# Kernel tuning notes

Measured on AMD Instinct MI355X. Metric: run time of the kernel, lower is better.

Reference implementation:

```python
import jax, jax.numpy as jnp
import numpy as np

# Fixed hierarchical grouping of the 15 regions into 5 groups of 3 (from split_regions)
SPLIT_IDX = np.array([[0, 1, 8], [2, 4, 6], [3, 5, 7], [9, 11, 13], [10, 12, 14]])
BN_EPS = 1e-5


def _bn_relu(x, g, b):
    # BatchNorm over (batch, spatial) dims in training-stats mode, then ReLU
    mu = jnp.mean(x, axis=(0, 2, 3), keepdims=True)
    var = jnp.var(x, axis=(0, 2, 3), keepdims=True)
    xn = (x - mu) * jax.lax.rsqrt(var + BN_EPS)
    return jax.nn.relu(xn * g[None, :, None, None] + b[None, :, None, None])


def _local_agg(x, params):
    # x: [B, Cin, G, K]; pointwise conv (1x1) -> BN -> ReLU per layer, then max over K
    for W, g, b in params:
        x = jnp.einsum('oi,bigk->bogk', W, x)
        x = _bn_relu(x, g, b)
    return jnp.max(x, axis=-1)  # [B, Cout, G]


def setup_inputs() -> dict:
    key = jax.random.key(0)
    ks = jax.random.split(key, 8)
    B, G, K = 32, 15, 2048
    inp = {"local_regions": jax.random.normal(ks[0], (B, G, K, 3), jnp.float32)}
    chans = [(3, 64, 64), (67, 128, 128), (131, 256, 256)]
    ki = 1
    for li, (c0, c1, c2) in enumerate(chans):
        for wi, (co, ci) in enumerate([(c1, c0), (c2, c1)]):
            inp[f"la{li}_w{wi}"] = jax.random.normal(ks[ki], (co, ci), jnp.float32) * (1.0 / np.sqrt(ci))
            inp[f"la{li}_g{wi}"] = jnp.ones((co,), jnp.float32)
            inp[f"la{li}_b{wi}"] = jnp.zeros((co,), jnp.float32)
            ki += 1
    return inp


def reference(local_regions,
              la0_w0, la0_g0, la0_b0, la0_w1, la0_g1, la0_b1,
              la1_w0, la1_g0, la1_b0, la1_w1, la1_g1, la1_b1,
              la2_w0, la2_g0, la2_b0, la2_w1, la2_g1, la2_b1):
    la0 = [(la0_w0, la0_g0, la0_b0), (la0_w1, la0_g1, la0_b1)]
    la1 = [(la1_w0, la1_g0, la1_b0), (la1_w1, la1_g1, la1_b1)]
    la2 = [(la2_w0, la2_g0, la2_b0), (la2_w1, la2_g1, la2_b1)]
    idx = jnp.asarray(SPLIT_IDX)

    x = jnp.transpose(local_regions, (0, 3, 1, 2))  # [B, 3, 15, K]
    centroids_1 = jnp.mean(x, axis=-1)              # [B, 3, 15]
    relative_1 = x - centroids_1[..., None]
    lf1 = _local_agg(relative_1, la0)               # [B, 64, 15]
    local_features = jnp.concatenate([centroids_1, lf1], axis=1)  # [B, 67, 15]

    # level 2: regroup 15 regions into [5, 3]
    lf1_s = jnp.transpose(lf1, (0, 2, 1))[:, idx, :]         # [B, 5, 3, 64]
    lr2 = jnp.transpose(centroids_1, (0, 2, 1))[:, idx, :]   # [B, 5, 3, 3]
    c2 = jnp.mean(lr2, axis=2)                               # [B, 5, 3]
    rel2 = lr2 - c2[:, :, None, :]
    feats2 = jnp.concatenate([rel2, lf1_s], axis=-1)         # [B, 5, 3, 67]
    feats2 = jnp.transpose(feats2, (0, 3, 1, 2))             # [B, 67, 5, 3]
    lf2 = _local_agg(feats2, la1)                            # [B, 128, 5]

    # level 3: global
    c3 = jnp.mean(c2, axis=1)                                # [B, 3]
    rel3 = c2 - c3[:, None, :]                               # [B, 5, 3]
    lf2 = jnp.concatenate([jnp.transpose(rel3, (0, 2, 1)), lf2], axis=1)  # [B, 131, 5]
    lf2 = lf2[:, :, None, :]                                 # [B, 131, 1, 5]
    gf = _local_agg(lf2, la2)                                # [B, 256, 1]
    return gf.squeeze(2), local_features
```

## Files before the change

kernel.cpp:

```cpp
#include <hip/hip_runtime.h>
#include <math.h>

#define BB 32
#define GG 15
#define KK 2048
#define NB 480
#define N1F 983040.0f
#define EPS 1e-5f
#define PZN ((int)0xAAAAAAAA)

typedef _Float16 half8 __attribute__((ext_vector_type(8)));
typedef float f32x4 __attribute__((ext_vector_type(4)));

#define WS_CENT  0
#define WS_MN    1920
#define GSREL    63360
#define GBN1     63600
#define G2A      67440
#define G2B      67952
#define G3A      68464
#define G3B      69488
#define FSREL    70512
#define FBN1     70520
#define F2A      70648
#define F2B      70904
#define F3A      71160
#define F3B      71672
#define CNT_GRP  72184
#define CNT_SUP  72376
#define CNT_DONE 72382

#define SMEMF 7936

__device__ const int SIDX[15] = {0,1,8, 2,4,6, 3,5,7, 9,11,13, 10,12,14};

__device__ __forceinline__ float wave_sum(float v){
    for (int off = 32; off; off >>= 1) v += __shfl_down(v, off, 64);
    return v;
}
__device__ __forceinline__ float aloadf(const float* p){
    return __hip_atomic_load(p, __ATOMIC_RELAXED, __HIP_MEMORY_SCOPE_AGENT);
}
__device__ __forceinline__ int aloadi(const int* p){
    return __hip_atomic_load(p, __ATOMIC_RELAXED, __HIP_MEMORY_SCOPE_AGENT);
}
template<int SLP, class Fold>
__device__ __forceinline__ void gbar(int* wsi, int idx, int gi, int ngrp,
                                     int* sflag, Fold fold){
    __syncthreads();
    if (threadIdx.x == 0)
        sflag[0] = (atomicAdd(&wsi[CNT_GRP + idx*32 + gi], 1) == PZN + 15) ? 1 : 0;
    __syncthreads();
    if (sflag[0]) {
        if (threadIdx.x == 0)
            sflag[1] = (atomicAdd(&wsi[CNT_SUP + idx], 1) == PZN + ngrp - 1) ? 1 : 0;
        __syncthreads();
        if (sflag[1]) {
            fold();
            __syncthreads();
            if (threadIdx.x == 0) atomicExch(&wsi[CNT_DONE + idx], 1);
        }
    }
    if (threadIdx.x == 0) {
        int g = 0;
        while (aloadi(&wsi[CNT_DONE + idx]) != 1 && ++g < 4000000)
            __builtin_amdgcn_s_sleep(SLP);
    }
    __syncthreads();
    asm volatile("" ::: "memory");
}

__global__ void __launch_bounds__(256, 2) mega(
        const float* __restrict__ x,
        const float* __restrict__ w00, const float* __restrict__ g00, const float* __restrict__ b00,
        const float* __restrict__ w01, const float* __restrict__ g01, const float* __restrict__ b01,
        const float* __restrict__ w10, const float* __restrict__ g10, const float* __restrict__ b10,
        const float* __restrict__ w11, const float* __restrict__ g11, const float* __restrict__ b11,
        const float* __restrict__ w20, const float* __restrict__ g20, const float* __restrict__ b20,
        const float* __restrict__ w21, const float* __restrict__ g21, const float* __restrict__ b21,
        float* __restrict__ ws, float* __restrict__ out) {
    __shared__ __align__(16) float smemf[SMEMF];
    float* xls  = smemf;
    float* redM = smemf + 6144; float* redN = smemf + 6400;
    float* redS = smemf + 6656; float* redQ = smemf + 6912;
    float* bcast= smemf + 7168;
    int*   sflag= (int*)(smemf + 7916);
    float* s1ls  = smemf;
    float* t1ls  = smemf + 64;
    float* centls= smemf + 128;
    float* c2ls  = smemf + 176;
    float* c3ls  = smemf + 192;
    float* f2ls  = smemf + 256;
    float* vls   = smemf + 1280;
    float* f3ls  = smemf + 3200;
    float* u3ls  = smemf + 3968;
    int* wsi = (int*)ws;

    int bid = blockIdx.x, tid = threadIdx.x;
    int b_ = bid / GG, g_ = bid % GG;
    int wv = tid >> 6, lane = tid & 63, l15 = lane & 15, quad = lane >> 4;
    int gi = bid >> 4;

    {
        const float4* xp4 = (const float4*)(x + (size_t)bid * KK * 3);
        float4* xls4 = (float4*)xls;
        #pragma unroll
        for (int i = 0; i < 6; i++) xls4[i*256 + tid] = xp4[i*256 + tid];
        __syncthreads();
        float m[9] = {0,0,0,0,0,0,0,0,0};
        float a[24];
        const float* bp = &xls[tid*24];
        #pragma unroll
        for (int i = 0; i < 6; i++)
            *reinterpret_cast<float4*>(&a[i*4]) = *reinterpret_cast<const float4*>(&bp[i*4]);
        #pragma unroll
        for (int p = 0; p < 8; p++) {
            float ax=a[p*3], ay=a[p*3+1], az=a[p*3+2];
            m[0]+=ax; m[1]+=ay; m[2]+=az;
            m[3]=fmaf(ax,ax,m[3]); m[4]=fmaf(ay,ay,m[4]); m[5]=fmaf(az,az,m[5]);
            m[6]=fmaf(ax,ay,m[6]); m[7]=fmaf(ax,az,m[7]); m[8]=fmaf(ay,az,m[8]);
        }
        #pragma unroll
        for (int q = 0; q < 9; q++) {
            float v = wave_sum(m[q]);
            if (lane == 0) redM[q*4 + wv] = v;
        }
        __syncthreads();
        if (tid == 0) {
            float t[9];
            #pragma unroll
            for (int q = 0; q < 9; q++) t[q] = redM[q*4]+redM[q*4+1]+redM[q*4+2]+redM[q*4+3];
            float c0 = t[0]/KK, c1 = t[1]/KK, c2 = t[2]/KK;
            bcast[0]=c0; bcast[1]=c1; bcast[2]=c2;
            out[8192 + b_*(67*GG) + 0*GG + g_] = c0;
            out[8192 + b_*(67*GG) + 1*GG + g_] = c1;
            out[8192 + b_*(67*GG) + 2*GG + g_] = c2;
            atomicExch(&ws[WS_CENT + bid*4 + 0], c0);
            atomicExch(&ws[WS_CENT + bid*4 + 1], c1);
            atomicExch(&ws[WS_CENT + bid*4 + 2], c2);
            redM[40] = t[3] - KK*c0*c0;  redM[41] = t[4] - KK*c1*c1;
            redM[42] = t[5] - KK*c2*c2;  redM[43] = t[6] - KK*c0*c1;
            redM[44] = t[7] - KK*c0*c2;  redM[45] = t[8] - KK*c1*c2;
        }
        __syncthreads();
    }
    if (tid < 6) atomicAdd(&ws[GSREL + gi*8 + tid], redM[40 + tid]);

    half8 afA[4], afB[4];
    #pragma unroll
    for (int t = 0; t < 4; t++)
        #pragma unroll
        for (int j = 0; j < 8; j++) {
            afA[t][j] = (_Float16)w01[(t*16 + l15)*64 + quad*8 + j];
            afB[t][j] = (_Float16)w01[(t*16 + l15)*64 + 32 + quad*8 + j];
        }
    gbar<8>(wsi, 0, gi, 30, sflag, [&]{
        if (tid < 6) {
            float acc = 0.f;
            #pragma unroll
            for (int s = 0; s < 30; s++) acc += aloadf(&ws[GSREL + s*8 + tid]);
            atomicExch(&ws[FSREL + tid], acc);
        }
    });

    if (tid < 6) bcast[3+tid] = aloadf(&ws[FSREL + tid]) / N1F;
    __syncthreads();
    float c0 = bcast[0], c1 = bcast[1], c2v = bcast[2];
    float S00=bcast[3], S11=bcast[4], S22=bcast[5], S01=bcast[6], S02=bcast[7], S12=bcast[8];

    float wa0[8], wa1[8], wa2[8], ba[8], wb0[8], wb1[8], wb2[8], bb[8];
    #pragma unroll
    for (int j = 0; j < 8; j++) {
        int cA = quad*8 + j;
        float u0=w00[cA*3+0], u1=w00[cA*3+1], u2=w00[cA*3+2];
        float var = u0*u0*S00 + u1*u1*S11 + u2*u2*S22
                  + 2.f*(u0*u1*S01 + u0*u2*S02 + u1*u2*S12);
        float a1 = g00[cA]*rsqrtf(var + EPS);
        wa0[j]=a1*u0; wa1[j]=a1*u1; wa2[j]=a1*u2; ba[j]=b00[cA];
        int cB = cA + 32;
        float v0=w00[cB*3+0], v1=w00[cB*3+1], v2=w00[cB*3+2];
        float varB = v0*v0*S00 + v1*v1*S11 + v2*v2*S22
                   + 2.f*(v0*v1*S01 + v0*v2*S02 + v1*v2*S12);
        float a1B = g00[cB]*rsqrtf(varB + EPS);
        wb0[j]=a1B*v0; wb1[j]=a1B*v1; wb2[j]=a1B*v2; bb[j]=b00[cB];
    }
    float mx[16], mn[16], sm[16], sq[16];
    #pragma unroll
    for (int s = 0; s < 16; s++) { mx[s]=-1e30f; mn[s]=1e30f; sm[s]=0.f; sq[s]=0.f; }

    for (int it = 0; it < 32; it++) {
        int k = it*64 + wv*16 + l15;
        float r0 = xls[k*3+0]-c0, r1 = xls[k*3+1]-c1, r2 = xls[k*3+2]-c2v;
        half8 bf0, bf1;
        #pragma unroll
        for (int j = 0; j < 8; j++) {
            float pA = fmaf(wa0[j],r0, fmaf(wa1[j],r1, fmaf(wa2[j],r2, ba[j])));
            bf0[j] = (_Float16)fmaxf(pA, 0.f);
            float pB = fmaf(wb0[j],r0, fmaf(wb1[j],r1, fmaf(wb2[j],r2, bb[j])));
            bf1[j] = (_Float16)fmaxf(pB, 0.f);
        }
        #pragma unroll
        for (int t = 0; t < 4; t++) {
            f32x4 acc = {0.f,0.f,0.f,0.f};
            acc = __builtin_amdgcn_mfma_f32_16x16x32_f16(afA[t], bf0, acc, 0, 0, 0);
            acc = __builtin_amdgcn_mfma_f32_16x16x32_f16(afB[t], bf1, acc, 0, 0, 0);
            #pragma unroll
            for (int r = 0; r < 4; r++) {
                float h = acc[r];
                int s = t*4 + r;
                mx[s]=fmaxf(mx[s],h); mn[s]=fminf(mn[s],h);
                sm[s]+=h;             sq[s]=fmaf(h,h,sq[s]);
            }
        }
    }
    #pragma unroll
    for (int m = 1; m < 16; m <<= 1) {
        #pragma unroll
        for (int s = 0; s < 16; s++) {
            mx[s] = fmaxf(mx[s], __shfl_xor(mx[s], m, 64));
            mn[s] = fminf(mn[s], __shfl_xor(mn[s], m, 64));
            sm[s] += __shfl_xor(sm[s], m, 64);
            sq[s] += __shfl_xor(sq[s], m, 64);
        }
    }
    __syncthreads();
    if (l15 == 0) {
        #pragma unroll
        for (int t = 0; t < 4; t++)
            #pragma unroll
            for (int r = 0; r < 4; r++) {
                int o = t*16 + quad*4 + r;
                redM[wv*64+o]=mx[t*4+r]; redN[wv*64+o]=mn[t*4+r];
                redS[wv*64+o]=sm[t*4+r]; redQ[wv*64+o]=sq[t*4+r];
            }
    }
    __syncthreads();
    float Mreg = -1e30f, Nreg = 1e30f;
    if (tid < 64) {
        float S=0.f, Q=0.f;
        #pragma unroll
        for (int w = 0; w < 4; w++) {
            Mreg = fmaxf(Mreg, redM[w*64+tid]); Nreg = fminf(Nreg, redN[w*64+tid]);
            S += redS[w*64+tid];               Q += redQ[w*64+tid];
        }
        atomicAdd(&ws[GBN1 + gi*128 + tid], S);
        atomicAdd(&ws[GBN1 + gi*128 + 64 + tid], Q);
        atomicExch(&ws[WS_MN + bid*128 + tid], Mreg);
        atomicExch(&ws[WS_MN + bid*128 + 64 + tid], Nreg);
    }
    gbar<8>(wsi, 1, gi, 30, sflag, [&]{
        if (tid < 128) {
            float acc = 0.f;
            #pragma unroll
            for (int s = 0; s < 30; s++) acc += aloadf(&ws[GBN1 + s*128 + tid]);
            atomicExch(&ws[FBN1 + tid], acc);
        }
    });

    if (tid < 64) {
        float SM = aloadf(&ws[FBN1 + tid]);
        float SQ = aloadf(&ws[FBN1 + 64 + tid]);
        float mean = SM / N1F;
        float var  = SQ / N1F - mean*mean;
        float s1 = g01[tid]*rsqrtf(var + EPS);
        float t1 = b01[tid] - mean*s1;
        float val = fmaxf(fmaf(s1, (s1 >= 0.f) ? Mreg : Nreg, t1), 0.f);
        out[8192 + b_*(67*GG) + (3+tid)*GG + g_] = val;
        s1ls[tid] = s1; t1ls[tid] = t1;
    }
    if (g_ != 0) return;

    int git = b_ >> 4;
    if (tid < 45) centls[tid] = aloadf(&ws[WS_CENT + (b_*GG + tid/3)*4 + tid%3]);
    __syncthreads();
    if (tid < 15) {
        int s = tid/3, i = tid%3;
        c2ls[tid] = (centls[SIDX[s*3+0]*3+i] + centls[SIDX[s*3+1]*3+i]
                   + centls[SIDX[s*3+2]*3+i]) * (1.f/3.f);
    }
    __syncthreads();
    if (tid < 3)
        c3ls[tid] = (c2ls[tid]+c2ls[3+tid]+c2ls[6+tid]+c2ls[9+tid]+c2ls[12+tid]) * 0.2f;
    if (tid < 45) {
        int p = tid/3, i = tid%3;
        f2ls[p*68 + i] = centls[SIDX[p]*3+i] - c2ls[(p/3)*3 + i];
    }
    for (int u = tid; u < 960; u += 256) {
        int p = u >> 6, ch = u & 63, gsrc = SIDX[p];
        float Mv = aloadf(&ws[WS_MN + (b_*GG + gsrc)*128 + ch]);
        float Nv = aloadf(&ws[WS_MN + (b_*GG + gsrc)*128 + 64 + ch]);
        float s1 = s1ls[ch], t1 = t1ls[ch];
        f2ls[p*68 + 3 + ch] = fmaxf(fmaf(s1, (s1 >= 0.f) ? Mv : Nv, t1), 0.f);
    }
    __syncthreads();

    int half = tid >> 7, oc = tid & 127, pbase = half*8, npts = 8 - half;
    float acc[8];
    #pragma unroll
    for (int q = 0; q < 8; q++) acc[q] = 0.f;
    {
        const float* wr = w10 + oc*67;
        #pragma unroll 4
        for (int c = 0; c < 67; c++) {
            float wv_ = wr[c];
            #pragma unroll
            for (int q = 0; q < 8; q++)
                acc[q] = fmaf(wv_, f2ls[(pbase+q)*68 + c], acc[q]);
        }
        float S = 0.f, Q = 0.f;
        #pragma unroll
        for (int q = 0; q < 8; q++) if (q < npts) { S += acc[q]; Q = fmaf(acc[q],acc[q],Q); }
        redS[tid] = S; redQ[tid] = Q;
        __syncthreads();
        if (tid < 128) {
            atomicAdd(&ws[G2A + git*256 + tid],       redS[tid] + redS[tid+128]);
            atomicAdd(&ws[G2A + git*256 + 128 + tid], redQ[tid] + redQ[tid+128]);
        }
    }
    gbar<2>(wsi, 2, git, 2, sflag, [&]{
        float a = aloadf(&ws[G2A + tid]) + aloadf(&ws[G2A + 256 + tid]);
        atomicExch(&ws[F2A + tid], a);
    });

    {
        float mean = aloadf(&ws[F2A + oc]) / 480.f;
        float var  = aloadf(&ws[F2A + 128 + oc]) / 480.f - mean*mean;
        float s2 = g10[oc]*rsqrtf(var + EPS), t2 = b10[oc] - mean*s2;
        #pragma unroll
        for (int q = 0; q < 8; q++) {
            float v = fmaxf(fmaf(s2, acc[q], t2), 0.f);
            if (q < npts) vls[(pbase+q)*128 + oc] = v;
        }
    }
    __syncthreads();
    #pragma unroll
    for (int q = 0; q < 8; q++) acc[q] = 0.f;
    {
        const float* wr = w11 + oc*128;
        #pragma unroll 4
        for (int c = 0; c < 128; c++) {
            float wv_ = wr[c];
            #pragma unroll
            for (int q = 0; q < 8; q++)
                acc[q] = fmaf(wv_, vls[(pbase+q)*128 + c], acc[q]);
        }
        float S = 0.f, Q = 0.f;
        #pragma unroll
        for (int q = 0; q < 8; q++) if (q < npts) { S += acc[q]; Q = fmaf(acc[q],acc[q],Q); }
        redS[tid] = S; redQ[tid] = Q;
        __syncthreads();
        if (tid < 128) {
            atomicAdd(&ws[G2B + git*256 + tid],       redS[tid] + redS[tid+128]);
            atomicAdd(&ws[G2B + git*256 + 128 + tid], redQ[tid] + redQ[tid+128]);
        }
    }
    gbar<2>(wsi, 3, git, 2, sflag, [&]{
        float a = aloadf(&ws[G2B + tid]) + aloadf(&ws[G2B + 256 + tid]);
        atomicExch(&ws[F2B + tid], a);
    });

    {
        float mean = aloadf(&ws[F2B + oc]) / 480.f;
        float var  = aloadf(&ws[F2B + 128 + oc]) / 480.f - mean*mean;
        float s3 = g11[oc]*rsqrtf(var + EPS), t3 = b11[oc] - mean*s3;
        #pragma unroll
        for (int q = 0; q < 8; q++) {
            float v = fmaxf(fmaf(s3, acc[q], t3), 0.f);
            if (q < npts) vls[(pbase+q)*128 + oc] = v;
        }
    }
    __syncthreads();
    for (int u = tid; u < 640; u += 256) {
        int s = u >> 7, o2 = u & 127;
        float m = fmaxf(fmaxf(vls[(3*s)*128+o2], vls[(3*s+1)*128+o2]),
                        vls[(3*s+2)*128+o2]);
        f3ls[s*132 + 3 + o2] = m;
    }
    if (tid < 15) {
        int s = tid/3, i = tid%3;
        f3ls[s*132 + i] = c2ls[tid] - c3ls[i];
    }
    __syncthreads();

    float a3[5];
    #pragma unroll
    for (int s = 0; s < 5; s++) a3[s] = 0.f;
    {
        const float* wr = w20 + tid*131;
        #pragma unroll 4
        for (int c = 0; c < 131; c++) {
            float wv_ = wr[c];
            #pragma unroll
            for (int s = 0; s < 5; s++)
                a3[s] = fmaf(wv_, f3ls[s*132 + c], a3[s]);
        }
        float S = 0.f, Q = 0.f;
        #pragma unroll
        for (int s = 0; s < 5; s++) { S += a3[s]; Q = fmaf(a3[s],a3[s],Q); }
        atomicAdd(&ws[G3A + git*512 + tid], S);
        atomicAdd(&ws[G3A + git*512 + 256 + tid], Q);
    }
    gbar<2>(wsi, 4, git, 2, sflag, [&]{
        float a0 = aloadf(&ws[G3A + tid])       + aloadf(&ws[G3A + 512 + tid]);
        float a1 = aloadf(&ws[G3A + 256 + tid]) + aloadf(&ws[G3A + 512 + 256 + tid]);
        atomicExch(&ws[F3A + tid], a0);
        atomicExch(&ws[F3A + 256 + tid], a1);
    });

    {
        float mean = aloadf(&ws[F3A + tid]) / 160.f;
        float var  = aloadf(&ws[F3A + 256 + tid]) / 160.f - mean*mean;
        float s4 = g20[tid]*rsqrtf(var + EPS), t4 = b20[tid] - mean*s4;
        #pragma unroll
        for (int s = 0; s < 5; s++)
            u3ls[s*256 + tid] = fmaxf(fmaf(s4, a3[s], t4), 0.f);
    }
    __syncthreads();
    #pragma unroll
    for (int s = 0; s < 5; s++) a3[s] = 0.f;
    {
        const float* wr = w21 + tid*256;
        #pragma unroll 4
        for (int c = 0; c < 256; c++) {
            float wv_ = wr[c];
            #pragma unroll
            for (int s = 0; s < 5; s++)
                a3[s] = fmaf(wv_, u3ls[s*256 + c], a3[s]);
        }
        float S = 0.f, Q = 0.f;
        #pragma unroll
        for (int s = 0; s < 5; s++) { S += a3[s]; Q = fmaf(a3[s],a3[s],Q); }
        atomicAdd(&ws[G3B + git*512 + tid], S);
        atomicAdd(&ws[G3B + git*512 + 256 + tid], Q);
    }
    gbar<2>(wsi, 5, git, 2, sflag, [&]{
        float a0 = aloadf(&ws[G3B + tid])       + aloadf(&ws[G3B + 512 + tid]);
        float a1 = aloadf(&ws[G3B + 256 + tid]) + aloadf(&ws[G3B + 512 + 256 + tid]);
        atomicExch(&ws[F3B + tid], a0);
        atomicExch(&ws[F3B + 256 + tid], a1);
    });

    {
        float mean = aloadf(&ws[F3B + tid]) / 160.f;
        float var  = aloadf(&ws[F3B + 256 + tid]) / 160.f - mean*mean;
        float s5 = g21[tid]*rsqrtf(var + EPS), t5 = b21[tid] - mean*s5;
        float m = -1e30f;
        #pragma unroll
        for (int s = 0; s < 5; s++)
            m = fmaxf(m, fmaxf(fmaf(s5, a3[s], t5), 0.f));
        out[b_*256 + tid] = m;
    }
}

extern "C" void kernel_launch(void* const* d_in, const int* in_sizes, int n_in,
                              void* d_out, int out_size, void* d_ws, size_t ws_size,
                              hipStream_t stream) {
    (void)in_sizes; (void)n_in; (void)out_size; (void)ws_size;
    const float* x   = (const float*)d_in[0];
    const float* w00 = (const float*)d_in[1];
    const float* g00 = (const float*)d_in[2];
    const float* b00 = (const float*)d_in[3];
    const float* w01 = (const float*)d_in[4];
    const float* g01 = (const float*)d_in[5];
    const float* b01 = (const float*)d_in[6];
    const float* w10 = (const float*)d_in[7];
    const float* g10 = (const float*)d_in[8];
    const float* b10 = (const float*)d_in[9];
    const float* w11 = (const float*)d_in[10];
    const float* g11 = (const float*)d_in[11];
    const float* b11 = (const float*)d_in[12];
    const float* w20 = (const float*)d_in[13];
    const float* g20 = (const float*)d_in[14];
    const float* b20 = (const float*)d_in[15];
    const float* w21 = (const float*)d_in[16];
    const float* g21 = (const float*)d_in[17];
    const float* b21 = (const float*)d_in[18];
    float* out = (float*)d_out;
    float* ws  = (float*)d_ws;

    mega<<<NB, 256, 0, stream>>>(x, w00,g00,b00, w01,g01,b01, w10,g10,b10,
                                 w11,g11,b11, w20,g20,b20, w21,g21,b21, ws, out);
}
```

Baseline: 191.1 us.

## Split persistent megakernel with spin barriers into chain of stream-ordered kernels

Replaces the single persistent kernel, which used atomic counters and spin-wait grid barriers between BatchNorm stages, with eight separate kernel launches. Global statistics are now written as per-block partials and reduced deterministically by the next kernel, with no atomics. Level-2/3 activations are stored in the workspace and recomputed or reloaded across launches. This removes spin-barrier latency and atomic contention at the cost of several extra launch overheads and redundant recomputation, such as re-reading x and recomputing level-2 features.

```diff
diff --git a/kernel.cpp b/kernel.cpp
--- a/kernel.cpp
+++ b/kernel.cpp
@@ -1,36 +1,27 @@
 #include <hip/hip_runtime.h>
 #include <math.h>
 
-#define BB 32
 #define GG 15
 #define KK 2048
 #define NB 480
 #define N1F 983040.0f
 #define EPS 1e-5f
-#define PZN ((int)0xAAAAAAAA)
 
 typedef _Float16 half8 __attribute__((ext_vector_type(8)));
 typedef float f32x4 __attribute__((ext_vector_type(4)));
 
-#define WS_CENT  0
-#define WS_MN    1920
-#define GSREL    63360
-#define GBN1     63600
-#define G2A      67440
-#define G2B      67952
-#define G3A      68464
-#define G3B      69488
-#define FSREL    70512
-#define FBN1     70520
-#define F2A      70648
-#define F2B      70904
-#define F3A      71160
-#define F3B      71672
-#define CNT_GRP  72184
-#define CNT_SUP  72376
-#define CNT_DONE 72382
-
-#define SMEMF 7936
+#define CENT  0
+#define MOM   1920
+#define SELO  5760
+#define SQ1   36480
+#define H2BO  36480
+#define H3AO  97920
+#define H3BO  5760
+#define P2A   138880
+#define P2B   147072
+#define P3A   155264
+#define P3B   171648
+#define COEF1 188032
 
 __device__ const int SIDX[15] = {0,1,8, 2,4,6, 3,5,7, 9,11,13, 10,12,14};
 
@@ -38,114 +29,86 @@
     for (int off = 32; off; off >>= 1) v += __shfl_down(v, off, 64);
     return v;
 }
-__device__ __forceinline__ float aloadf(const float* p){
-    return __hip_atomic_load(p, __ATOMIC_RELAXED, __HIP_MEMORY_SCOPE_AGENT);
-}
-__device__ __forceinline__ int aloadi(const int* p){
-    return __hip_atomic_load(p, __ATOMIC_RELAXED, __HIP_MEMORY_SCOPE_AGENT);
-}
-template<int SLP, class Fold>
-__device__ __forceinline__ void gbar(int* wsi, int idx, int gi, int ngrp,
-                                     int* sflag, Fold fold){
-    __syncthreads();
-    if (threadIdx.x == 0)
-        sflag[0] = (atomicAdd(&wsi[CNT_GRP + idx*32 + gi], 1) == PZN + 15) ? 1 : 0;
-    __syncthreads();
-    if (sflag[0]) {
-        if (threadIdx.x == 0)
-            sflag[1] = (atomicAdd(&wsi[CNT_SUP + idx], 1) == PZN + ngrp - 1) ? 1 : 0;
-        __syncthreads();
-        if (sflag[1]) {
-            fold();
-            __syncthreads();
-            if (threadIdx.x == 0) atomicExch(&wsi[CNT_DONE + idx], 1);
-        }
-    }
-    if (threadIdx.x == 0) {
-        int g = 0;
-        while (aloadi(&wsi[CNT_DONE + idx]) != 1 && ++g < 4000000)
-            __builtin_amdgcn_s_sleep(SLP);
-    }
-    __syncthreads();
-    asm volatile("" ::: "memory");
-}
-
-__global__ void __launch_bounds__(256, 2) mega(
+
+__global__ __launch_bounds__(256) void k1_moments(
+        const float* __restrict__ x, float* __restrict__ ws, float* __restrict__ out){
+    __shared__ __align__(16) float xls[6144];
+    __shared__ float red[40];
+    int bid = blockIdx.x, tid = threadIdx.x;
+    int b_ = bid / GG, g_ = bid % GG;
+    int wv = tid >> 6, lane = tid & 63;
+    const float4* xp4 = (const float4*)(x + (size_t)bid * KK * 3);
+    float4* xls4 = (float4*)xls;
+    #pragma unroll
+    for (int i = 0; i < 6; i++) xls4[i*256 + tid] = xp4[i*256 + tid];
+    __syncthreads();
+    float m[9] = {0,0,0,0,0,0,0,0,0};
+    float a[24];
+    const float* bp = &xls[tid*24];
+    #pragma unroll
+    for (int i = 0; i < 6; i++)
+        *reinterpret_cast<float4*>(&a[i*4]) = *reinterpret_cast<const float4*>(&bp[i*4]);
+    #pragma unroll
+    for (int p = 0; p < 8; p++) {
+        float ax=a[p*3], ay=a[p*3+1], az=a[p*3+2];
+        m[0]+=ax; m[1]+=ay; m[2]+=az;
+        m[3]=fmaf(ax,ax,m[3]); m[4]=fmaf(ay,ay,m[4]); m[5]=fmaf(az,az,m[5]);
+        m[6]=fmaf(ax,ay,m[6]); m[7]=fmaf(ax,az,m[7]); m[8]=fmaf(ay,az,m[8]);
+    }
+    #pragma unroll
+    for (int q = 0; q < 9; q++) {
+        float v = wave_sum(m[q]);
+        if (lane == 0) red[q*4 + wv] = v;
+    }
+    __syncthreads();
+    if (tid == 0) {
+        float t[9];
+        #pragma unroll
+        for (int q = 0; q < 9; q++) t[q] = red[q*4]+red[q*4+1]+red[q*4+2]+red[q*4+3];
+        float c0 = t[0]/KK, c1 = t[1]/KK, c2 = t[2]/KK;
+        out[8192 + b_*1005 + 0*GG + g_] = c0;
+        out[8192 + b_*1005 + 1*GG + g_] = c1;
+        out[8192 + b_*1005 + 2*GG + g_] = c2;
+        ws[CENT + bid*4 + 0] = c0;
+        ws[CENT + bid*4 + 1] = c1;
+        ws[CENT + bid*4 + 2] = c2;
+        ws[MOM + bid*8 + 0] = t[3] - KK*c0*c0;
+        ws[MOM + bid*8 + 1] = t[4] - KK*c1*c1;
+        ws[MOM + bid*8 + 2] = t[5] - KK*c2*c2;
+        ws[MOM + bid*8 + 3] = t[6] - KK*c0*c1;
+        ws[MOM + bid*8 + 4] = t[7] - KK*c0*c2;
+        ws[MOM + bid*8 + 5] = t[8] - KK*c1*c2;
+    }
+}
+
+__global__ __launch_bounds__(256, 2) void k3_mfma(
         const float* __restrict__ x,
-        const float* __restrict__ w00, const float* __restrict__ g00, const float* __restrict__ b00,
-        const float* __restrict__ w01, const float* __restrict__ g01, const float* __restrict__ b01,
-        const float* __restrict__ w10, const float* __restrict__ g10, const float* __restrict__ b10,
-        const float* __restrict__ w11, const float* __restrict__ g11, const float* __restrict__ b11,
-        const float* __restrict__ w20, const float* __restrict__ g20, const float* __restrict__ b20,
-        const float* __restrict__ w21, const float* __restrict__ g21, const float* __restrict__ b21,
-        float* __restrict__ ws, float* __restrict__ out) {
-    __shared__ __align__(16) float smemf[SMEMF];
+        const float* __restrict__ w00, const float* __restrict__ g00,
+        const float* __restrict__ b00, const float* __restrict__ w01,
+        const float* __restrict__ g01, float* __restrict__ ws){
+    __shared__ __align__(16) float smemf[7440];
     float* xls  = smemf;
     float* redM = smemf + 6144; float* redN = smemf + 6400;
     float* redS = smemf + 6656; float* redQ = smemf + 6912;
     float* bcast= smemf + 7168;
-    int*   sflag= (int*)(smemf + 7916);
-    float* s1ls  = smemf;
-    float* t1ls  = smemf + 64;
-    float* centls= smemf + 128;
-    float* c2ls  = smemf + 176;
-    float* c3ls  = smemf + 192;
-    float* f2ls  = smemf + 256;
-    float* vls   = smemf + 1280;
-    float* f3ls  = smemf + 3200;
-    float* u3ls  = smemf + 3968;
-    int* wsi = (int*)ws;
+    float* sred = smemf + 7184;
 
     int bid = blockIdx.x, tid = threadIdx.x;
-    int b_ = bid / GG, g_ = bid % GG;
     int wv = tid >> 6, lane = tid & 63, l15 = lane & 15, quad = lane >> 4;
-    int gi = bid >> 4;
 
     {
         const float4* xp4 = (const float4*)(x + (size_t)bid * KK * 3);
         float4* xls4 = (float4*)xls;
         #pragma unroll
         for (int i = 0; i < 6; i++) xls4[i*256 + tid] = xp4[i*256 + tid];
-        __syncthreads();
-        float m[9] = {0,0,0,0,0,0,0,0,0};
-        float a[24];
-        const float* bp = &xls[tid*24];
-        #pragma unroll
-        for (int i = 0; i < 6; i++)
-            *reinterpret_cast<float4*>(&a[i*4]) = *reinterpret_cast<const float4*>(&bp[i*4]);
-        #pragma unroll
-        for (int p = 0; p < 8; p++) {
-            float ax=a[p*3], ay=a[p*3+1], az=a[p*3+2];
-            m[0]+=ax; m[1]+=ay; m[2]+=az;
-            m[3]=fmaf(ax,ax,m[3]); m[4]=fmaf(ay,ay,m[4]); m[5]=fmaf(az,az,m[5]);
-            m[6]=fmaf(ax,ay,m[6]); m[7]=fmaf(ax,az,m[7]); m[8]=fmaf(ay,az,m[8]);
-        }
-        #pragma unroll
-        for (int q = 0; q < 9; q++) {
-            float v = wave_sum(m[q]);
-            if (lane == 0) redM[q*4 + wv] = v;
-        }
-        __syncthreads();
-        if (tid == 0) {
-            float t[9];
-            #pragma unroll
-            for (int q = 0; q < 9; q++) t[q] = redM[q*4]+redM[q*4+1]+redM[q*4+2]+redM[q*4+3];
-            float c0 = t[0]/KK, c1 = t[1]/KK, c2 = t[2]/KK;
-            bcast[0]=c0; bcast[1]=c1; bcast[2]=c2;
-            out[8192 + b_*(67*GG) + 0*GG + g_] = c0;
-            out[8192 + b_*(67*GG) + 1*GG + g_] = c1;
-            out[8192 + b_*(67*GG) + 2*GG + g_] = c2;
-            atomicExch(&ws[WS_CENT + bid*4 + 0], c0);
-            atomicExch(&ws[WS_CENT + bid*4 + 1], c1);
-            atomicExch(&ws[WS_CENT + bid*4 + 2], c2);
-            redM[40] = t[3] - KK*c0*c0;  redM[41] = t[4] - KK*c1*c1;
-            redM[42] = t[5] - KK*c2*c2;  redM[43] = t[6] - KK*c0*c1;
-            redM[44] = t[7] - KK*c0*c2;  redM[45] = t[8] - KK*c1*c2;
-        }
-        __syncthreads();
-    }
-    if (tid < 6) atomicAdd(&ws[GSREL + gi*8 + tid], redM[40 + tid]);
-
+    }
+    float sacc = 0.f;
+    {
+        int c = tid >> 3, q = tid & 7;
+        #pragma unroll
+        for (int i = 0; i < 15; i++) sacc += ws[MOM + (c*15 + i)*8 + q];
+    }
+    float cload = (tid < 3) ? ws[CENT + bid*4 + tid] : 0.f;
     half8 afA[4], afB[4];
     #pragma unroll
     for (int t = 0; t < 4; t++)
@@ -154,16 +117,15 @@
             afA[t][j] = (_Float16)w01[(t*16 + l15)*64 + quad*8 + j];
             afB[t][j] = (_Float16)w01[(t*16 + l15)*64 + 32 + quad*8 + j];
         }
-    gbar<8>(wsi, 0, gi, 30, sflag, [&]{
-        if (tid < 6) {
-            float acc = 0.f;
-            #pragma unroll
-            for (int s = 0; s < 30; s++) acc += aloadf(&ws[GSREL + s*8 + tid]);
-            atomicExch(&ws[FSREL + tid], acc);
-        }
-    });
-
-    if (tid < 6) bcast[3+tid] = aloadf(&ws[FSREL + tid]) / N1F;
+    sred[tid] = sacc;
+    __syncthreads();
+    if (tid < 6) {
+        float tot = 0.f;
+        #pragma unroll
+        for (int c = 0; c < 32; c++) tot += sred[c*8 + tid];
+        bcast[3 + tid] = tot / N1F;
+    }
+    if (tid < 3) bcast[tid] = cload;
     __syncthreads();
     float c0 = bcast[0], c1 = bcast[1], c2v = bcast[2];
     float S00=bcast[3], S11=bcast[4], S22=bcast[5], S01=bcast[6], S02=bcast[7], S12=bcast[8];
@@ -224,7 +186,7 @@
         }
     }
     __syncthreads();
-    if (l15 == 0) {
+    if ((lane & 15) == 0) {
         #pragma unroll
         for (int t = 0; t < 4; t++)
             #pragma unroll
@@ -235,65 +197,140 @@
             }
     }
     __syncthreads();
-    float Mreg = -1e30f, Nreg = 1e30f;
     if (tid < 64) {
-        float S=0.f, Q=0.f;
+        float Mreg = -1e30f, Nreg = 1e30f, S=0.f, Q=0.f;
         #pragma unroll
         for (int w = 0; w < 4; w++) {
             Mreg = fmaxf(Mreg, redM[w*64+tid]); Nreg = fminf(Nreg, redN[w*64+tid]);
             S += redS[w*64+tid];               Q += redQ[w*64+tid];
         }
-        atomicAdd(&ws[GBN1 + gi*128 + tid], S);
-        atomicAdd(&ws[GBN1 + gi*128 + 64 + tid], Q);
-        atomicExch(&ws[WS_MN + bid*128 + tid], Mreg);
-        atomicExch(&ws[WS_MN + bid*128 + 64 + tid], Nreg);
-    }
-    gbar<8>(wsi, 1, gi, 30, sflag, [&]{
-        if (tid < 128) {
-            float acc = 0.f;
-            #pragma unroll
-            for (int s = 0; s < 30; s++) acc += aloadf(&ws[GBN1 + s*128 + tid]);
-            atomicExch(&ws[FBN1 + tid], acc);
-        }
-    });
-
+        ws[SELO + bid*64 + tid] = (g01[tid] >= 0.f) ? Mreg : Nreg;
+        ws[SQ1 + bid*128 + tid] = S;
+        ws[SQ1 + bid*128 + 64 + tid] = Q;
+    }
+}
+
+__global__ __launch_bounds__(256) void k_bn1red(
+        const float* __restrict__ g01, const float* __restrict__ b01,
+        float* __restrict__ ws){
+    __shared__ float sm[256];
+    int tid = threadIdx.x;
+    int e = tid & 127, h = tid >> 7;
+    float acc = 0.f;
+    #pragma unroll 8
+    for (int i = 0; i < 240; i++) acc += ws[SQ1 + (h*240 + i)*128 + e];
+    sm[tid] = acc;
+    __syncthreads();
     if (tid < 64) {
-        float SM = aloadf(&ws[FBN1 + tid]);
-        float SQ = aloadf(&ws[FBN1 + 64 + tid]);
-        float mean = SM / N1F;
-        float var  = SQ / N1F - mean*mean;
+        float S = sm[tid] + sm[128 + tid];
+        float Q = sm[64 + tid] + sm[192 + tid];
+        float mean = S / N1F;
+        float var  = Q / N1F - mean*mean;
         float s1 = g01[tid]*rsqrtf(var + EPS);
         float t1 = b01[tid] - mean*s1;
-        float val = fmaxf(fmaf(s1, (s1 >= 0.f) ? Mreg : Nreg, t1), 0.f);
-        out[8192 + b_*(67*GG) + (3+tid)*GG + g_] = val;
-        s1ls[tid] = s1; t1ls[tid] = t1;
-    }
-    if (g_ != 0) return;
-
-    int git = b_ >> 4;
-    if (tid < 45) centls[tid] = aloadf(&ws[WS_CENT + (b_*GG + tid/3)*4 + tid%3]);
+        ws[COEF1 + tid] = s1;
+        ws[COEF1 + 64 + tid] = t1;
+    }
+}
+
+__global__ __launch_bounds__(256) void k_t1(
+        const float* __restrict__ w10, float* __restrict__ ws,
+        float* __restrict__ out){
+    __shared__ float s1t1[128];
+    __shared__ float cent[48];
+    __shared__ float c2[16];
+    __shared__ __align__(16) float f2[16*68];
+    __shared__ float red[512];
+    int b = blockIdx.x, tid = threadIdx.x;
+    if (tid < 128) s1t1[tid] = ws[COEF1 + tid];
+    if (tid < 45) cent[tid] = ws[CENT + (b*GG + tid/3)*4 + tid%3];
+    if (tid >= 188) f2[15*68 + (tid - 188)] = 0.f;
     __syncthreads();
     if (tid < 15) {
         int s = tid/3, i = tid%3;
-        c2ls[tid] = (centls[SIDX[s*3+0]*3+i] + centls[SIDX[s*3+1]*3+i]
-                   + centls[SIDX[s*3+2]*3+i]) * (1.f/3.f);
-    }
-    __syncthreads();
-    if (tid < 3)
-        c3ls[tid] = (c2ls[tid]+c2ls[3+tid]+c2ls[6+tid]+c2ls[9+tid]+c2ls[12+tid]) * 0.2f;
+        c2[tid] = (cent[SIDX[s*3+0]*3+i] + cent[SIDX[s*3+1]*3+i]
+                 + cent[SIDX[s*3+2]*3+i]) * (1.f/3.f);
+    }
+    __syncthreads();
     if (tid < 45) {
         int p = tid/3, i = tid%3;
-        f2ls[p*68 + i] = centls[SIDX[p]*3+i] - c2ls[(p/3)*3 + i];
+        f2[p*68 + i] = cent[SIDX[p]*3+i] - c2[(p/3)*3 + i];
     }
     for (int u = tid; u < 960; u += 256) {
-        int p = u >> 6, ch = u & 63, gsrc = SIDX[p];
-        float Mv = aloadf(&ws[WS_MN + (b_*GG + gsrc)*128 + ch]);
-        float Nv = aloadf(&ws[WS_MN + (b_*GG + gsrc)*128 + 64 + ch]);
-        float s1 = s1ls[ch], t1 = t1ls[ch];
-        f2ls[p*68 + 3 + ch] = fmaxf(fmaf(s1, (s1 >= 0.f) ? Mv : Nv, t1), 0.f);
-    }
-    __syncthreads();
-
+        int p = u >> 6, ch = u & 63, g = SIDX[p];
+        float sel = ws[SELO + (b*GG + g)*64 + ch];
+        float val = fmaxf(fmaf(s1t1[ch], sel, s1t1[64+ch]), 0.f);
+        f2[p*68 + 3 + ch] = val;
+        out[8192 + b*1005 + (3+ch)*GG + g] = val;
+    }
+    __syncthreads();
+    int half = tid >> 7, oc = tid & 127, pbase = half*8, npts = 8 - half;
+    float acc[8];
+    #pragma unroll
+    for (int q = 0; q < 8; q++) acc[q] = 0.f;
+    const float* wr = w10 + oc*67;
+    #pragma unroll 4
+    for (int c = 0; c < 67; c++) {
+        float wv_ = wr[c];
+        #pragma unroll
+        for (int q = 0; q < 8; q++)
+            acc[q] = fmaf(wv_, f2[(pbase+q)*68 + c], acc[q]);
+    }
+    float S = 0.f, Q = 0.f;
+    #pragma unroll
+    for (int q = 0; q < 8; q++) if (q < npts) { S += acc[q]; Q = fmaf(acc[q],acc[q],Q); }
+    red[tid] = S; red[256 + tid] = Q;
+    __syncthreads();
+    if (tid < 128) {
+        ws[P2A + b*256 + tid]       = red[tid] + red[128 + tid];
+        ws[P2A + b*256 + 128 + tid] = red[256 + tid] + red[256 + 128 + tid];
+    }
+}
+
+__global__ __launch_bounds__(256) void k_t2(
+        const float* __restrict__ w10, const float* __restrict__ g10,
+        const float* __restrict__ b10, const float* __restrict__ w11,
+        float* __restrict__ ws){
+    __shared__ float s1t1[128];
+    __shared__ float cent[48];
+    __shared__ float c2[16];
+    __shared__ __align__(16) float f2[16*68];
+    __shared__ __align__(16) float vls[16*128];
+    __shared__ float c2s[128], c2t[128];
+    __shared__ float red[512];
+    int b = blockIdx.x, tid = threadIdx.x;
+    if (tid < 128) {
+        float S = 0.f, Q = 0.f;
+        #pragma unroll
+        for (int i = 0; i < 32; i++) {
+            S += ws[P2A + i*256 + tid];
+            Q += ws[P2A + i*256 + 128 + tid];
+        }
+        float mean = S / 480.f, var = Q / 480.f - mean*mean;
+        float s2 = g10[tid]*rsqrtf(var + EPS);
+        c2s[tid] = s2; c2t[tid] = b10[tid] - mean*s2;
+        s1t1[tid] = ws[COEF1 + tid];
+        vls[15*128 + tid] = 0.f;
+    }
+    if (tid < 45) cent[tid] = ws[CENT + (b*GG + tid/3)*4 + tid%3];
+    if (tid >= 188) f2[15*68 + (tid - 188)] = 0.f;
+    __syncthreads();
+    if (tid < 15) {
+        int s = tid/3, i = tid%3;
+        c2[tid] = (cent[SIDX[s*3+0]*3+i] + cent[SIDX[s*3+1]*3+i]
+                 + cent[SIDX[s*3+2]*3+i]) * (1.f/3.f);
+    }
+    __syncthreads();
+    if (tid < 45) {
+        int p = tid/3, i = tid%3;
+        f2[p*68 + i] = cent[SIDX[p]*3+i] - c2[(p/3)*3 + i];
+    }
+    for (int u = tid; u < 960; u += 256) {
+        int p = u >> 6, ch = u & 63, g = SIDX[p];
+        float sel = ws[SELO + (b*GG + g)*64 + ch];
+        f2[p*68 + 3 + ch] = fmaxf(fmaf(s1t1[ch], sel, s1t1[64+ch]), 0.f);
+    }
+    __syncthreads();
     int half = tid >> 7, oc = tid & 127, pbase = half*8, npts = 8 - half;
     float acc[8];
     #pragma unroll
@@ -305,27 +342,11 @@
             float wv_ = wr[c];
             #pragma unroll
             for (int q = 0; q < 8; q++)
-                acc[q] = fmaf(wv_, f2ls[(pbase+q)*68 + c], acc[q]);
-        }
-        float S = 0.f, Q = 0.f;
-        #pragma unroll
-        for (int q = 0; q < 8; q++) if (q < npts) { S += acc[q]; Q = fmaf(acc[q],acc[q],Q); }
-        redS[tid] = S; redQ[tid] = Q;
-        __syncthreads();
-        if (tid < 128) {
-            atomicAdd(&ws[G2A + git*256 + tid],       redS[tid] + redS[tid+128]);
-            atomicAdd(&ws[G2A + git*256 + 128 + tid], redQ[tid] + redQ[tid+128]);
-        }
-    }
-    gbar<2>(wsi, 2, git, 2, sflag, [&]{
-        float a = aloadf(&ws[G2A + tid]) + aloadf(&ws[G2A + 256 + tid]);
-        atomicExch(&ws[F2A + tid], a);
-    });
-
+                acc[q] = fmaf(wv_, f2[(pbase+q)*68 + c], acc[q]);
+        }
+    }
     {
-        float mean = aloadf(&ws[F2A + oc]) / 480.f;
-        float var  = aloadf(&ws[F2A + 128 + oc]) / 480.f - mean*mean;
-        float s2 = g10[oc]*rsqrtf(var + EPS), t2 = b10[oc] - mean*s2;
+        float s2 = c2s[oc], t2 = c2t[oc];
         #pragma unroll
         for (int q = 0; q < 8; q++) {
             float v = fmaxf(fmaf(s2, acc[q], t2), 0.f);
@@ -333,123 +354,175 @@
         }
     }
     __syncthreads();
-    #pragma unroll
-    for (int q = 0; q < 8; q++) acc[q] = 0.f;
+    float acc2[8];
+    #pragma unroll
+    for (int q = 0; q < 8; q++) acc2[q] = 0.f;
     {
-        const float* wr = w11 + oc*128;
-        #pragma unroll 4
-        for (int c = 0; c < 128; c++) {
-            float wv_ = wr[c];
+        const float4* w4 = (const float4*)(w11 + oc*128);
+        #pragma unroll 2
+        for (int c4 = 0; c4 < 32; c4++) {
+            float4 wv4 = w4[c4];
+            int cb = c4*4;
             #pragma unroll
-            for (int q = 0; q < 8; q++)
-                acc[q] = fmaf(wv_, vls[(pbase+q)*128 + c], acc[q]);
-        }
+            for (int q = 0; q < 8; q++) {
+                const float* vrow = &vls[(pbase+q)*128];
+                acc2[q] = fmaf(wv4.x, vrow[cb+0], acc2[q]);
+                acc2[q] = fmaf(wv4.y, vrow[cb+1], acc2[q]);
+                acc2[q] = fmaf(wv4.z, vrow[cb+2], acc2[q]);
+                acc2[q] = fmaf(wv4.w, vrow[cb+3], acc2[q]);
+            }
+        }
+    }
+    float S = 0.f, Q = 0.f;
+    #pragma unroll
+    for (int q = 0; q < 8; q++) if (q < npts) {
+        ws[H2BO + b*1920 + (pbase+q)*128 + oc] = acc2[q];
+        S += acc2[q]; Q = fmaf(acc2[q],acc2[q],Q);
+    }
+    red[tid] = S; red[256 + tid] = Q;
+    __syncthreads();
+    if (tid < 128) {
+        ws[P2B + b*256 + tid]       = red[tid] + red[128 + tid];
+        ws[P2B + b*256 + 128 + tid] = red[256 + tid] + red[256 + 128 + tid];
+    }
+}
+
+__global__ __launch_bounds__(256) void k_t3(
+        const float* __restrict__ g11, const float* __restrict__ b11,
+        const float* __restrict__ w20, float* __restrict__ ws){
+    __shared__ float s3[128], t3[128];
+    __shared__ float cent[48];
+    __shared__ float c2[16], c3[4];
+    __shared__ __align__(16) float f3[5*132];
+    int b = blockIdx.x, tid = threadIdx.x;
+    if (tid < 128) {
         float S = 0.f, Q = 0.f;
         #pragma unroll
-        for (int q = 0; q < 8; q++) if (q < npts) { S += acc[q]; Q = fmaf(acc[q],acc[q],Q); }
-        redS[tid] = S; redQ[tid] = Q;
-        __syncthreads();
-        if (tid < 128) {
-            atomicAdd(&ws[G2B + git*256 + tid],       redS[tid] + redS[tid+128]);
-            atomicAdd(&ws[G2B + git*256 + 128 + tid], redQ[tid] + redQ[tid+128]);
-        }
-    }
-    gbar<2>(wsi, 3, git, 2, sflag, [&]{
-        float a = aloadf(&ws[G2B + tid]) + aloadf(&ws[G2B + 256 + tid]);
-        atomicExch(&ws[F2B + tid], a);
-    });
-
-    {
-        float mean = aloadf(&ws[F2B + oc]) / 480.f;
-        float var  = aloadf(&ws[F2B + 128 + oc]) / 480.f - mean*mean;
-        float s3 = g11[oc]*rsqrtf(var + EPS), t3 = b11[oc] - mean*s3;
-        #pragma unroll
-        for (int q = 0; q < 8; q++) {
-            float v = fmaxf(fmaf(s3, acc[q], t3), 0.f);
-            if (q < npts) vls[(pbase+q)*128 + oc] = v;
-        }
-    }
-    __syncthreads();
-    for (int u = tid; u < 640; u += 256) {
-        int s = u >> 7, o2 = u & 127;
-        float m = fmaxf(fmaxf(vls[(3*s)*128+o2], vls[(3*s+1)*128+o2]),
-                        vls[(3*s+2)*128+o2]);
-        f3ls[s*132 + 3 + o2] = m;
-    }
+        for (int i = 0; i < 32; i++) {
+            S += ws[P2B + i*256 + tid];
+            Q += ws[P2B + i*256 + 128 + tid];
+        }
+        float mean = S / 480.f, var = Q / 480.f - mean*mean;
+        float sv = g11[tid]*rsqrtf(var + EPS);
+        s3[tid] = sv; t3[tid] = b11[tid] - mean*sv;
+    }
+    if (tid < 45) cent[tid] = ws[CENT + (b*GG + tid/3)*4 + tid%3];
+    __syncthreads();
     if (tid < 15) {
         int s = tid/3, i = tid%3;
-        f3ls[s*132 + i] = c2ls[tid] - c3ls[i];
-    }
-    __syncthreads();
-
+        c2[tid] = (cent[SIDX[s*3+0]*3+i] + cent[SIDX[s*3+1]*3+i]
+                 + cent[SIDX[s*3+2]*3+i]) * (1.f/3.f);
+    }
+    __syncthreads();
+    if (tid < 3)
+        c3[tid] = (c2[tid]+c2[3+tid]+c2[6+tid]+c2[9+tid]+c2[12+tid]) * 0.2f;
+    __syncthreads();
+    if (tid < 15) {
+        int s = tid/3, i = tid%3;
+        f3[s*132 + i] = c2[tid] - c3[i];
+    }
+    for (int u = tid; u < 640; u += 256) {
+        int s = u >> 7, ch = u & 127;
+        float sv = s3[ch], tv = t3[ch];
+        float m = -1e30f;
+        #pragma unroll
+        for (int j = 0; j < 3; j++) {
+            float hv = ws[H2BO + b*1920 + (3*s + j)*128 + ch];
+            m = fmaxf(m, fmaxf(fmaf(sv, hv, tv), 0.f));
+        }
+        f3[s*132 + 3 + ch] = m;
+    }
+    __syncthreads();
     float a3[5];
     #pragma unroll
     for (int s = 0; s < 5; s++) a3[s] = 0.f;
+    const float* wr = w20 + tid*131;
+    #pragma unroll 4
+    for (int c = 0; c < 131; c++) {
+        float wv_ = wr[c];
+        #pragma unroll
+        for (int s = 0; s < 5; s++)
+            a3[s] = fmaf(wv_, f3[s*132 + c], a3[s]);
+    }
+    float S = 0.f, Q = 0.f;
+    #pragma unroll
+    for (int s = 0; s < 5; s++) {
+        ws[H3AO + b*1280 + s*256 + tid] = a3[s];
+        S += a3[s]; Q = fmaf(a3[s],a3[s],Q);
+    }
+    ws[P3A + b*512 + tid] = S;
+    ws[P3A + b*512 + 256 + tid] = Q;
+}
+
+__global__ __launch_bounds__(256) void k_t4(
+        const float* __restrict__ g20, const float* __restrict__ b20,
+        const float* __restrict__ w21, float* __restrict__ ws){
+    __shared__ __align__(16) float u3ls[5*256];
+    int b = blockIdx.x, tid = threadIdx.x;
     {
-        const float* wr = w20 + tid*131;
-        #pragma unroll 4
-        for (int c = 0; c < 131; c++) {
-            float wv_ = wr[c];
-            #pragma unroll
-            for (int s = 0; s < 5; s++)
-                a3[s] = fmaf(wv_, f3ls[s*132 + c], a3[s]);
-        }
         float S = 0.f, Q = 0.f;
         #pragma unroll
-        for (int s = 0; s < 5; s++) { S += a3[s]; Q = fmaf(a3[s],a3[s],Q); }
-        atomicAdd(&ws[G3A + git*512 + tid], S);
-        atomicAdd(&ws[G3A + git*512 + 256 + tid], Q);
-    }
-    gbar<2>(wsi, 4, git, 2, sflag, [&]{
-        float a0 = aloadf(&ws[G3A + tid])       + aloadf(&ws[G3A + 512 + tid]);
-        float a1 = aloadf(&ws[G3A + 256 + tid]) + aloadf(&ws[G3A + 512 + 256 + tid]);
-        atomicExch(&ws[F3A + tid], a0);
-        atomicExch(&ws[F3A + 256 + tid], a1);
-    });
-
-    {
-        float mean = aloadf(&ws[F3A + tid]) / 160.f;
-        float var  = aloadf(&ws[F3A + 256 + tid]) / 160.f - mean*mean;
-        float s4 = g20[tid]*rsqrtf(var + EPS), t4 = b20[tid] - mean*s4;
-        #pragma unroll
-        for (int s = 0; s < 5; s++)
-            u3ls[s*256 + tid] = fmaxf(fmaf(s4, a3[s], t4), 0.f);
-    }
-    __syncthreads();
+        for (int i = 0; i < 32; i++) {
+            S += ws[P3A + i*512 + tid];
+            Q += ws[P3A + i*512 + 256 + tid];
+        }
+        float mean = S / 160.f, var = Q / 160.f - mean*mean;
+        float s4 = g20[tid]*rsqrtf(var + EPS);
+        float t4 = b20[tid] - mean*s4;
+        #pragma unroll
+        for (int s = 0; s < 5; s++) {
+            float hv = ws[H3AO + b*1280 + s*256 + tid];
+            u3ls[s*256 + tid] = fmaxf(fmaf(s4, hv, t4), 0.f);
+        }
+    }
+    __syncthreads();
+    float a3[5];
     #pragma unroll
     for (int s = 0; s < 5; s++) a3[s] = 0.f;
-    {
-        const float* wr = w21 + tid*256;
-        #pragma unroll 4
-        for (int c = 0; c < 256; c++) {
-            float wv_ = wr[c];
-            #pragma unroll
-            for (int s = 0; s < 5; s++)
-                a3[s] = fmaf(wv_, u3ls[s*256 + c], a3[s]);
-        }
-        float S = 0.f, Q = 0.f;
-        #pragma unroll
-        for (int s = 0; s < 5; s++) { S += a3[s]; Q = fmaf(a3[s],a3[s],Q); }
-        atomicAdd(&ws[G3B + git*512 + tid], S);
-        atomicAdd(&ws[G3B + git*512 + 256 + tid], Q);
-    }
-    gbar<2>(wsi, 5, git, 2, sflag, [&]{
-        float a0 = aloadf(&ws[G3B + tid])       + aloadf(&ws[G3B + 512 + tid]);
-        float a1 = aloadf(&ws[G3B + 256 + tid]) + aloadf(&ws[G3B + 512 + 256 + tid]);
-        atomicExch(&ws[F3B + tid], a0);
-        atomicExch(&ws[F3B + 256 + tid], a1);
-    });
-
-    {
-        float mean = aloadf(&ws[F3B + tid]) / 160.f;
-        float var  = aloadf(&ws[F3B + 256 + tid]) / 160.f - mean*mean;
-        float s5 = g21[tid]*rsqrtf(var + EPS), t5 = b21[tid] - mean*s5;
-        float m = -1e30f;
-        #pragma unroll
-        for (int s = 0; s < 5; s++)
-            m = fmaxf(m, fmaxf(fmaf(s5, a3[s], t5), 0.f));
-        out[b_*256 + tid] = m;
-    }
+    const float4* w4 = (const float4*)(w21 + tid*256);
+    #pragma unroll 2
+    for (int c4 = 0; c4 < 64; c4++) {
+        float4 wv4 = w4[c4];
+        int cb = c4*4;
+        #pragma unroll
+        for (int s = 0; s < 5; s++) {
+            const float* ur = &u3ls[s*256];
+            a3[s] = fmaf(wv4.x, ur[cb+0], a3[s]);
+            a3[s] = fmaf(wv4.y, ur[cb+1], a3[s]);
+            a3[s] = fmaf(wv4.z, ur[cb+2], a3[s]);
+            a3[s] = fmaf(wv4.w, ur[cb+3], a3[s]);
+        }
+    }
+    float S = 0.f, Q = 0.f;
+    #pragma unroll
+    for (int s = 0; s < 5; s++) {
+        ws[H3BO + b*1280 + s*256 + tid] = a3[s];
+        S += a3[s]; Q = fmaf(a3[s],a3[s],Q);
+    }
+    ws[P3B + b*512 + tid] = S;
+    ws[P3B + b*512 + 256 + tid] = Q;
+}
+
+__global__ __launch_bounds__(256) void k_t5(
+        const float* __restrict__ g21, const float* __restrict__ b21,
+        float* __restrict__ ws, float* __restrict__ out){
+    int b = blockIdx.x, tid = threadIdx.x;
+    float S = 0.f, Q = 0.f;
+    #pragma unroll
+    for (int i = 0; i < 32; i++) {
+        S += ws[P3B + i*512 + tid];
+        Q += ws[P3B + i*512 + 256 + tid];
+    }
+    float mean = S / 160.f, var = Q / 160.f - mean*mean;
+    float s5 = g21[tid]*rsqrtf(var + EPS);
+    float t5 = b21[tid] - mean*s5;
+    float m = -1e30f;
+    #pragma unroll
+    for (int s = 0; s < 5; s++) {
+        float hv = ws[H3BO + b*1280 + s*256 + tid];
+        m = fmaxf(m, fmaxf(fmaf(s5, hv, t5), 0.f));
+    }
+    out[b*256 + tid] = m;
 }
 
 extern "C" void kernel_launch(void* const* d_in, const int* in_sizes, int n_in,
@@ -478,6 +551,12 @@
     float* out = (float*)d_out;
     float* ws  = (float*)d_ws;
 
-    mega<<<NB, 256, 0, stream>>>(x, w00,g00,b00, w01,g01,b01, w10,g10,b10,
-                                 w11,g11,b11, w20,g20,b20, w21,g21,b21, ws, out);
-}
+    k1_moments<<<NB, 256, 0, stream>>>(x, ws, out);
+    k3_mfma  <<<NB, 256, 0, stream>>>(x, w00, g00, b00, w01, g01, ws);
+    k_bn1red <<<1,  256, 0, stream>>>(g01, b01, ws);
+    k_t1     <<<32, 256, 0, stream>>>(w10, ws, out);
+    k_t2     <<<32, 256, 0, stream>>>(w10, g10, b10, w11, ws);
+    k_t3     <<<32, 256, 0, stream>>>(g11, b11, w20, ws);
+    k_t4     <<<32, 256, 0, stream>>>(g20, b20, w21, ws);
+    k_t5     <<<32, 256, 0, stream>>>(g21, b21, ws, out);
+}
```

Result: slower. 205.6 us (+7.6%).
